# Optimization experiments

Measured on AMD Instinct MI355X. Metric: run time of the kernel, lower is better.

## Reference

```python
import jax, jax.numpy as jnp
import numpy as np
from jax import lax

MAX_ITER = 15
EPS_ITER = 1e-6


def _div_no_nan(a, b):
    # tf.math.divide_no_nan: 0 where denominator is 0
    b_safe = jnp.where(b == 0, 1.0, b)
    return jnp.where(b == 0, 0.0, a / b_safe)


def _sinkhorn_iter(x):
    u = jnp.sum(x, axis=-2, keepdims=True)   # column sums [B,1,N]
    h = _div_no_nan(x, u)
    v = jnp.sum(h, axis=-1, keepdims=True)   # row sums    [B,N,1]
    return _div_no_nan(h, v)


def setup_inputs() -> dict:
    key = jax.random.key(0)
    x = jax.random.uniform(key, (128, 256, 256), dtype=jnp.float32)
    return {"x": x}


def reference(x):
    def cond(state):
        _, i, d = state
        return jnp.logical_and(i < MAX_ITER, d)

    def body(state):
        x, i, _ = state
        y = _sinkhorn_iter(x)
        diff = jnp.linalg.norm(y - x, axis=(-2, -1))  # per-matrix Frobenius norm
        d = jnp.any(diff >= EPS_ITER)
        return (y, i + 1, d)

    init = (x, jnp.int32(0), jnp.bool_(True))
    out, _, _ = lax.while_loop(cond, body, init)
    return out
```

## Files before the change

### kernel.cpp

```cpp
#include <hip/hip_runtime.h>


#define SK_ITERS 15

__global__ __launch_bounds__(1024, 4)
void sinkhorn_kernel(const float* __restrict__ x, float* __restrict__ out) {
    const int tid = threadIdx.x;
    const int tr  = tid >> 5;
    const int tc  = tid & 31;
    const int swz = tc >> 2;

    const float* __restrict__ xb = x   + (size_t)blockIdx.x * 65536;
    float*       __restrict__ ob = out + (size_t)blockIdx.x * 65536;

    __shared__ float partA[32][256];
    __shared__ float part2[4][256];
    __shared__ float urcp[256];

    float v[8][8];
#pragma unroll
    for (int i = 0; i < 8; ++i) {
        const float4* p = (const float4*)(xb + (tr * 8 + i) * 256 + tc * 8);
        float4 a = p[0];
        float4 b = p[1];
        v[i][0] = a.x; v[i][1] = a.y; v[i][2] = a.z; v[i][3] = a.w;
        v[i][4] = b.x; v[i][5] = b.y; v[i][6] = b.z; v[i][7] = b.w;
    }

    const int c2   = tid & 255;
    const int q2   = tid >> 8;
    const int idx2 = (c2 & ~7) | ((c2 & 7) ^ ((c2 >> 5) & 7));

    for (int it = 0; it < SK_ITERS; ++it) {
#pragma unroll
        for (int j = 0; j < 8; ++j) {
            float s = v[0][j] + v[1][j] + v[2][j] + v[3][j]
                    + v[4][j] + v[5][j] + v[6][j] + v[7][j];
            partA[tr][tc * 8 + (j ^ swz)] = s;
        }
        __syncthreads();

        {
            float s = 0.f;
#pragma unroll
            for (int p = 0; p < 8; ++p) s += partA[q2 * 8 + p][idx2];
            part2[q2][c2] = s;
        }
        __syncthreads();

        if (tid < 256) {
            float s = part2[0][tid] + part2[1][tid] + part2[2][tid] + part2[3][tid];
            float r = (s == 0.f) ? 0.f : __builtin_amdgcn_rcpf(s);
            int w = (tid & ~7) | ((tid & 7) ^ ((tid >> 5) & 7));
            urcp[w] = r;
        }
        __syncthreads();

        float ur[8];
#pragma unroll
        for (int j = 0; j < 8; ++j) ur[j] = urcp[tc * 8 + (j ^ swz)];

        float rs[8];
#pragma unroll
        for (int i = 0; i < 8; ++i) {
            float s = 0.f;
#pragma unroll
            for (int j = 0; j < 8; ++j) {
                v[i][j] *= ur[j];
                s += v[i][j];
            }
            rs[i] = s;
        }

#pragma unroll
        for (int m = 16; m >= 1; m >>= 1) {
#pragma unroll
            for (int i = 0; i < 8; ++i) rs[i] += __shfl_xor(rs[i], m, 32);
        }

#pragma unroll
        for (int i = 0; i < 8; ++i) {
            float r = (rs[i] == 0.f) ? 0.f : __builtin_amdgcn_rcpf(rs[i]);
#pragma unroll
            for (int j = 0; j < 8; ++j) v[i][j] *= r;
        }
    }

#pragma unroll
    for (int i = 0; i < 8; ++i) {
        float4* p = (float4*)(ob + (tr * 8 + i) * 256 + tc * 8);
        float4 a, b;
        a.x = v[i][0]; a.y = v[i][1]; a.z = v[i][2]; a.w = v[i][3];
        b.x = v[i][4]; b.y = v[i][5]; b.z = v[i][6]; b.w = v[i][7];
        p[0] = a;
        p[1] = b;
    }
}

extern "C" void kernel_launch(void* const* d_in, const int* in_sizes, int n_in,
                              void* d_out, int out_size, void* d_ws, size_t ws_size,
                              hipStream_t stream) {
    const float* x = (const float*)d_in[0];
    float* out = (float*)d_out;
    const int batches = in_sizes[0] / 65536;
    hipLaunchKernelGGL(sinkhorn_kernel, dim3(batches), dim3(1024), 0, stream,
                       x, out);
}
```

Measured before the change: 124.5 us.

## Track Sinkhorn row/column scaling vectors instead of rescaling the matrix each iteration

After: 195.8 us. 1.57x slower.

```diff
diff --git a/kernel.cpp b/kernel.cpp
--- a/kernel.cpp
+++ b/kernel.cpp
@@ -3,97 +3,105 @@
 
 #define SK_ITERS 15
 
+__device__ __forceinline__ float guarded_rcp(float s) {
+    return (s == 0.f) ? 0.f : __builtin_amdgcn_rcpf(s);
+}
+
 __global__ __launch_bounds__(1024, 4)
-void sinkhorn_kernel(const float* __restrict__ x, float* __restrict__ out) {
-    const int tid = threadIdx.x;
-    const int tr  = tid >> 5;
-    const int tc  = tid & 31;
-    const int swz = tc >> 2;
+void sinkhorn_kernel(const float* __restrict__ xg, float* __restrict__ outg) {
+    const int tid  = threadIdx.x;
+    const int tr   = tid >> 5;
+    const int tc   = tid & 31;
+    const int key  = tc >> 2;
+    const int wv   = tid >> 6;
+    const int half = (tid >> 5) & 1;
 
-    const float* __restrict__ xb = x   + (size_t)blockIdx.x * 65536;
-    float*       __restrict__ ob = out + (size_t)blockIdx.x * 65536;
+    const float* __restrict__ xb = xg   + (size_t)blockIdx.x * 65536;
+    float*       __restrict__ ob = outg + (size_t)blockIdx.x * 65536;
 
-    __shared__ float partA[32][256];
-    __shared__ float part2[4][256];
-    __shared__ float urcp[256];
+    __shared__ float partA[16][256];
+    __shared__ float brcp[256];
 
-    float v[8][8];
+    float x[8][8];
 #pragma unroll
     for (int i = 0; i < 8; ++i) {
         const float4* p = (const float4*)(xb + (tr * 8 + i) * 256 + tc * 8);
-        float4 a = p[0];
-        float4 b = p[1];
-        v[i][0] = a.x; v[i][1] = a.y; v[i][2] = a.z; v[i][3] = a.w;
-        v[i][4] = b.x; v[i][5] = b.y; v[i][6] = b.z; v[i][7] = b.w;
+        float4 u = p[0], w = p[1];
+        x[i][0] = u.x; x[i][1] = u.y; x[i][2] = u.z; x[i][3] = u.w;
+        x[i][4] = w.x; x[i][5] = w.y; x[i][6] = w.z; x[i][7] = w.w;
     }
 
-    const int c2   = tid & 255;
-    const int q2   = tid >> 8;
-    const int idx2 = (c2 & ~7) | ((c2 & 7) ^ ((c2 >> 5) & 7));
+    float a[8];
+#pragma unroll
+    for (int i = 0; i < 8; ++i) a[i] = 1.f;
+    float b[8];
+
+    const int fidx = (tid & ~7) | ((tid & 7) ^ ((tid >> 5) & 7));
 
     for (int it = 0; it < SK_ITERS; ++it) {
+        float p[8];
 #pragma unroll
         for (int j = 0; j < 8; ++j) {
-            float s = v[0][j] + v[1][j] + v[2][j] + v[3][j]
-                    + v[4][j] + v[5][j] + v[6][j] + v[7][j];
-            partA[tr][tc * 8 + (j ^ swz)] = s;
+            float s = a[0] * x[0][j];
+#pragma unroll
+            for (int i = 1; i < 8; ++i) s = fmaf(a[i], x[i][j], s);
+            p[j] = s;
         }
-        __syncthreads();
-
+#pragma unroll
+        for (int j = 0; j < 8; ++j) p[j] += __shfl_xor(p[j], 32, 64);
         {
-            float s = 0.f;
+            const int j0 = half * 4;
 #pragma unroll
-            for (int p = 0; p < 8; ++p) s += partA[q2 * 8 + p][idx2];
-            part2[q2][c2] = s;
+            for (int q = 0; q < 4; ++q) {
+                const int j = j0 + q;
+                partA[wv][tc * 8 + (j ^ key)] = p[j];
+            }
         }
         __syncthreads();
 
         if (tid < 256) {
-            float s = part2[0][tid] + part2[1][tid] + part2[2][tid] + part2[3][tid];
-            float r = (s == 0.f) ? 0.f : __builtin_amdgcn_rcpf(s);
-            int w = (tid & ~7) | ((tid & 7) ^ ((tid >> 5) & 7));
-            urcp[w] = r;
+            float t[16];
+#pragma unroll
+            for (int w = 0; w < 16; ++w) t[w] = partA[w][fidx];
+#pragma unroll
+            for (int st = 8; st >= 1; st >>= 1)
+#pragma unroll
+                for (int w = 0; w < st; ++w) t[w] += t[w + st];
+            brcp[fidx] = guarded_rcp(t[0]);
         }
         __syncthreads();
 
-        float ur[8];
 #pragma unroll
-        for (int j = 0; j < 8; ++j) ur[j] = urcp[tc * 8 + (j ^ swz)];
+        for (int j = 0; j < 8; ++j) b[j] = brcp[tc * 8 + (j ^ key)];
 
         float rs[8];
 #pragma unroll
         for (int i = 0; i < 8; ++i) {
-            float s = 0.f;
+            float s = x[i][0] * b[0];
 #pragma unroll
-            for (int j = 0; j < 8; ++j) {
-                v[i][j] *= ur[j];
-                s += v[i][j];
-            }
+            for (int j = 1; j < 8; ++j) s = fmaf(x[i][j], b[j], s);
             rs[i] = s;
         }
-
 #pragma unroll
         for (int m = 16; m >= 1; m >>= 1) {
 #pragma unroll
-            for (int i = 0; i < 8; ++i) rs[i] += __shfl_xor(rs[i], m, 32);
+            for (int i = 0; i < 8; ++i) rs[i] += __shfl_xor(rs[i], m, 64);
         }
-
 #pragma unroll
-        for (int i = 0; i < 8; ++i) {
-            float r = (rs[i] == 0.f) ? 0.f : __builtin_amdgcn_rcpf(rs[i]);
-#pragma unroll
-            for (int j = 0; j < 8; ++j) v[i][j] *= r;
-        }
+        for (int i = 0; i < 8; ++i) a[i] = guarded_rcp(rs[i]);
     }
 
 #pragma unroll
     for (int i = 0; i < 8; ++i) {
-        float4* p = (float4*)(ob + (tr * 8 + i) * 256 + tc * 8);
-        float4 a, b;
-        a.x = v[i][0]; a.y = v[i][1]; a.z = v[i][2]; a.w = v[i][3];
-        b.x = v[i][4]; b.y = v[i][5]; b.z = v[i][6]; b.w = v[i][7];
-        p[0] = a;
-        p[1] = b;
+        const float ai = a[i];
+        float4 u, w;
+        u.x = ai * x[i][0] * b[0]; u.y = ai * x[i][1] * b[1];
+        u.z = ai * x[i][2] * b[2]; u.w = ai * x[i][3] * b[3];
+        w.x = ai * x[i][4] * b[4]; w.y = ai * x[i][5] * b[5];
+        w.z = ai * x[i][6] * b[6]; w.w = ai * x[i][7] * b[7];
+        float4* po = (float4*)(ob + (tr * 8 + i) * 256 + tc * 8);
+        po[0] = u;
+        po[1] = w;
     }
 }
 
```
